# Kernel tuning notes

Measured on AMD Instinct MI355X. Metric: run time of the kernel, lower is better.

The kernel has to match this reference:

```python
import jax, jax.numpy as jnp
import numpy as np

B, K, T = 8192, 6, 30
HID, GRU_H, INTENT = 256, 256, 32


def setup_inputs() -> dict:
    key = jax.random.key(0)
    ks = jax.random.split(key, 11)
    s = lambda fan: 1.0 / np.sqrt(fan)
    return {
        "context": jax.random.normal(ks[0], (B, HID), jnp.float32),
        "goals": jax.random.normal(ks[1], (B, K, 2), jnp.float32),
        "intent_emb": jax.random.normal(ks[2], (B, INTENT), jnp.float32),
        "W_h0": jax.random.normal(ks[3], (GRU_H, HID + 2 + INTENT), jnp.float32) * s(HID + 34),
        "b_h0": jax.random.normal(ks[4], (GRU_H,), jnp.float32) * s(HID + 34),
        "W_ih": jax.random.normal(ks[5], (3 * GRU_H, 2), jnp.float32) * s(GRU_H),
        "W_hh": jax.random.normal(ks[6], (3 * GRU_H, GRU_H), jnp.float32) * s(GRU_H),
        "b_ih": jax.random.normal(ks[7], (3 * GRU_H,), jnp.float32) * s(GRU_H),
        "b_hh": jax.random.normal(ks[8], (3 * GRU_H,), jnp.float32) * s(GRU_H),
        "W_out": jax.random.normal(ks[9], (2, GRU_H), jnp.float32) * s(GRU_H),
        "b_out": jax.random.normal(ks[10], (2,), jnp.float32) * s(GRU_H),
    }


def reference(context, goals, intent_emb, W_h0, b_h0, W_ih, W_hh, b_ih, b_hh, W_out, b_out):
    Bq, Kq, _ = goals.shape
    H = W_hh.shape[1]
    # Fold modes into batch: init input is [context, goal_k, intent] per mode.
    ctx = jnp.broadcast_to(context[:, None, :], (Bq, Kq, context.shape[-1]))
    emb = jnp.broadcast_to(intent_emb[:, None, :], (Bq, Kq, intent_emb.shape[-1]))
    init_in = jnp.concatenate([ctx, goals, emb], axis=-1).reshape(Bq * Kq, -1)
    h0 = init_in @ W_h0.T + b_h0                       # (BK, H)
    pos0 = jnp.zeros((Bq * Kq, 2), dtype=context.dtype)

    def step(carry, _):
        h, prev = carry
        gi = prev @ W_ih.T + b_ih                      # (BK, 3H)
        gh = h @ W_hh.T + b_hh                         # (BK, 3H)
        i_r, i_z, i_n = jnp.split(gi, 3, axis=-1)
        h_r, h_z, h_n = jnp.split(gh, 3, axis=-1)
        r = jax.nn.sigmoid(i_r + h_r)
        z = jax.nn.sigmoid(i_z + h_z)
        n = jnp.tanh(i_n + r * h_n)
        h_new = (1.0 - z) * n + z * h
        delta = h_new @ W_out.T + b_out                # (BK, 2)
        pos = prev + delta
        return (h_new, pos), pos

    _, preds = jax.lax.scan(step, (h0, pos0), None, length=T)  # (T, BK, 2)
    preds = preds.transpose(1, 0, 2).reshape(Bq, Kq, T, 2)     # (B, K, T, 2)
    correction = goals - preds[:, :, -1, :]                    # (B, K, 2)
    scale = (jnp.arange(1, T + 1, dtype=preds.dtype) / T)      # (T,)
    return preds + correction[:, :, None, :] * scale[None, None, :, None]
```

## Files before the change

kernel.cpp:

```cpp
#include <hip/hip_runtime.h>


typedef __attribute__((ext_vector_type(8))) short short8;
typedef __bf16 bf16x8 __attribute__((ext_vector_type(8)));
typedef float f32x16 __attribute__((ext_vector_type(16)));
typedef float f32x4 __attribute__((ext_vector_type(4)));

#define HSTR 264
#define NSEQ_BLK 32
#define WHH3_ELEMS (24 * 16 * 64 * 8)
#define WH0_ELEMS (8 * 20 * 64 * 8)

static __device__ __forceinline__ unsigned short f2bf(float f) {
  unsigned u = __builtin_bit_cast(unsigned, f);
  u += 0x7fffu + ((u >> 16) & 1u);
  return (unsigned short)(u >> 16);
}
static __device__ __forceinline__ float bf2f(unsigned short h) {
  unsigned u = ((unsigned)h) << 16;
  return __builtin_bit_cast(float, u);
}
static __device__ __forceinline__ bf16x8 ldfrag(const unsigned short* p) {
  return __builtin_bit_cast(bf16x8, *(const short8*)p);
}
static __device__ __forceinline__ float fsig(float x) {
  return __builtin_amdgcn_rcpf(1.f + __builtin_amdgcn_exp2f(-1.44269504f * x));
}
static __device__ __forceinline__ float ftanh(float x) {
  return 1.f - 2.f * __builtin_amdgcn_rcpf(1.f + __builtin_amdgcn_exp2f(2.88539008f * x));
}
static __device__ __forceinline__ float dpp16sum(float x) {
  x += __builtin_bit_cast(float, __builtin_amdgcn_update_dpp(0, __builtin_bit_cast(int, x), 0xB1, 0xF, 0xF, true));
  x += __builtin_bit_cast(float, __builtin_amdgcn_update_dpp(0, __builtin_bit_cast(int, x), 0x4E, 0xF, 0xF, true));
  x += __builtin_bit_cast(float, __builtin_amdgcn_update_dpp(0, __builtin_bit_cast(int, x), 0x141, 0xF, 0xF, true));
  x += __builtin_bit_cast(float, __builtin_amdgcn_update_dpp(0, __builtin_bit_cast(int, x), 0x140, 0xF, 0xF, true));
  return x;
}
static __device__ __forceinline__ void bar_lgkm() {
  asm volatile("s_waitcnt lgkmcnt(0)\n\ts_barrier" ::: "memory");
}

__global__ void prep_whh3_k(const float* __restrict__ Whh, unsigned short* __restrict__ Whhp3) {
  int i = blockIdx.x * 256 + threadIdx.x;
  if (i >= WHH3_ELEMS) return;
  int j = i & 7;
  int lane = (i >> 3) & 63;
  int rest = i >> 9;
  int ks = rest & 15;
  int sw = rest >> 4;
  int g = sw >> 3, w = sw & 7;
  int row = g * 256 + w * 32 + (lane & 31);
  int k = ks * 16 + ((lane >> 5) << 3) + j;
  Whhp3[i] = f2bf(Whh[row * 256 + k]);
}

__global__ void prep_wh0_k(const float* __restrict__ Wh0, unsigned short* __restrict__ Wh0p) {
  int i = blockIdx.x * 256 + threadIdx.x;
  if (i >= WH0_ELEMS) return;
  int j = i & 7;
  int lane = (i >> 3) & 63;
  int rest = i >> 9;
  int ks = rest % 20;
  int nt = rest / 20;
  int row = nt * 32 + (lane & 31);
  int k = ks * 16 + ((lane >> 5) << 3) + j;
  float v = (k < 290) ? Wh0[row * 290 + k] : 0.f;
  Wh0p[i] = f2bf(v);
}

__global__ void prep_gp_k(const float* __restrict__ bih, const float* __restrict__ bhh,
                          const float* __restrict__ Wih, const float* __restrict__ Wout,
                          float* __restrict__ gpo) {
  int n = threadIdx.x;
  gpo[n * 12 + 0]  = bih[n] + bhh[n];
  gpo[n * 12 + 1]  = bih[n + 256] + bhh[n + 256];
  gpo[n * 12 + 2]  = bih[n + 512];
  gpo[n * 12 + 3]  = bhh[n + 512];
  gpo[n * 12 + 4]  = Wih[n * 2 + 0];
  gpo[n * 12 + 5]  = Wih[n * 2 + 1];
  gpo[n * 12 + 6]  = Wih[(n + 256) * 2 + 0];
  gpo[n * 12 + 7]  = Wih[(n + 256) * 2 + 1];
  gpo[n * 12 + 8]  = Wih[(n + 512) * 2 + 0];
  gpo[n * 12 + 9]  = Wih[(n + 512) * 2 + 1];
  gpo[n * 12 + 10] = Wout[n];
  gpo[n * 12 + 11] = Wout[256 + n];
}

__global__ __launch_bounds__(512, 2) void gru_main_k(
    const float* __restrict__ ctx, const float* __restrict__ goals,
    const float* __restrict__ emb, const float* __restrict__ bh0,
    const float* __restrict__ bout,
    const unsigned short* __restrict__ Wh0p,
    const unsigned short* __restrict__ Whhp3,
    const float* __restrict__ gp,
    float* __restrict__ out) {
  __shared__ __align__(16) unsigned short wNl[8 * 16 * 64 * 8];
  __shared__ __align__(16) unsigned short Hb[NSEQ_BLK * HSTR];
  __shared__ __align__(16) float dpart[16 * NSEQ_BLK * 2];
  __shared__ __align__(16) float posL[NSEQ_BLK * 2];

  const int tid = threadIdx.x;
  const int w = tid >> 6;
  const int l = tid & 63;
  const int l31 = l & 31;
  const int grp = l >> 5;
  const int seq0 = blockIdx.x * NSEQ_BLK;
  const int n0 = w * 32 + l31;

  {
    const short8* wsrc = (const short8*)(Whhp3 + 131072);
    short8* wdst = (short8*)wNl;
    for (int i = tid; i < 8192; i += 512) wdst[i] = wsrc[i];
  }
  bf16x8 wR[16], wZ[16];
#pragma unroll
  for (int ks = 0; ks < 16; ++ks) {
    wR[ks] = ldfrag(&Whhp3[(((0 * 8 + w) * 16 + ks) * 64 + l) * 8]);
    wZ[ks] = ldfrag(&Whhp3[(((1 * 8 + w) * 16 + ks) * 64 + l) * 8]);
  }

  f32x16 acc0 = f32x16{};
  unsigned short* As = Hb;
  for (int cc = 0; cc < 2; ++cc) {
    for (int i = tid; i < NSEQ_BLK * 160; i += 512) {
      int row = i / 160;
      int col = i - row * 160;
      int d = cc * 160 + col;
      int s = seq0 + row;
      int b = s / 6;
      float v;
      if (d < 256)      v = ctx[b * 256 + d];
      else if (d < 258) v = goals[s * 2 + (d - 256)];
      else if (d < 290) v = emb[b * 32 + (d - 258)];
      else              v = 0.f;
      As[row * 176 + col] = f2bf(v);
    }
    __syncthreads();
    for (int ks = 0; ks < 10; ++ks) {
      bf16x8 bf = ldfrag(&Wh0p[((w * 20 + cc * 10 + ks) * 64 + l) * 8]);
      bf16x8 af = ldfrag(&As[l31 * 176 + ks * 16 + grp * 8]);
      acc0 = __builtin_amdgcn_mfma_f32_32x32x16_bf16(af, bf, acc0, 0, 0, 0);
    }
    __syncthreads();
  }
  {
    float b0 = bh0[n0];
#pragma unroll
    for (int r = 0; r < 16; ++r) {
      int row = (r & 3) + 8 * (r >> 2) + 4 * grp;
      Hb[row * HSTR + n0] = f2bf(acc0[r] + b0);
    }
  }
  if (tid < 2 * NSEQ_BLK) posL[tid] = 0.f;

  float brr, bzz, bin_, bhn, wr0, wr1, wz0, wz1, wn0, wn1, wo0, wo1;
  {
    f32x4 g0 = *(const f32x4*)&gp[n0 * 12];
    f32x4 g1 = *(const f32x4*)&gp[n0 * 12 + 4];
    f32x4 g2 = *(const f32x4*)&gp[n0 * 12 + 8];
    brr = g0[0]; bzz = g0[1]; bin_ = g0[2]; bhn = g0[3];
    wr0 = g1[0]; wr1 = g1[1]; wz0 = g1[2]; wz1 = g1[3];
    wn0 = g2[0]; wn1 = g2[1]; wo0 = g2[2]; wo1 = g2[3];
  }
  const float bo0 = bout[0], bo1 = bout[1];
  __syncthreads();

  for (int t = 0; t < 30; ++t) {
    f32x16 ar = f32x16{}, az = f32x16{}, an = f32x16{};

#pragma unroll
    for (int ks = 0; ks < 16; ++ks) {
      bf16x8 af = ldfrag(&Hb[l31 * HSTR + ks * 16 + grp * 8]);
      bf16x8 bN = ldfrag(&wNl[((w * 16 + ks) * 64 + l) * 8]);
      ar = __builtin_amdgcn_mfma_f32_32x32x16_bf16(af, wR[ks], ar, 0, 0, 0);
      az = __builtin_amdgcn_mfma_f32_32x32x16_bf16(af, wZ[ks], az, 0, 0, 0);
      an = __builtin_amdgcn_mfma_f32_32x32x16_bf16(af, bN, an, 0, 0, 0);
    }
    bar_lgkm();

#pragma unroll
    for (int q2 = 0; q2 < 4; ++q2) {
      int sb = 8 * q2 + 4 * grp;
      f32x4 xyA = *(const f32x4*)&posL[sb * 2];
      f32x4 xyB = *(const f32x4*)&posL[sb * 2 + 4];
#pragma unroll
      for (int e = 0; e < 4; ++e) {
        int r = 4 * q2 + e;
        int s = sb + e;
        float x = (e == 0) ? xyA[0] : (e == 1) ? xyA[2] : (e == 2) ? xyB[0] : xyB[2];
        float y = (e == 0) ? xyA[1] : (e == 1) ? xyA[3] : (e == 2) ? xyB[1] : xyB[3];
        int ha = s * HSTR + n0;
        float h = bf2f(Hb[ha]);
        float rg = fsig(ar[r] + brr + x * wr0 + y * wr1);
        float zg = fsig(az[r] + bzz + x * wz0 + y * wz1);
        float ng = ftanh(fmaf(rg, an[r] + bhn, fmaf(x, wn0, fmaf(y, wn1, bin_))));
        float hnew = fmaf(zg, h - ng, ng);
        Hb[ha] = f2bf(hnew);
        float dx = dpp16sum(hnew * wo0);
        float dy = dpp16sum(hnew * wo1);
        if ((l & 15) == 0) {
          int p16 = w * 2 + ((l >> 4) & 1);
          dpart[(p16 * NSEQ_BLK + s) * 2]     = dx;
          dpart[(p16 * NSEQ_BLK + s) * 2 + 1] = dy;
        }
      }
    }
    bar_lgkm();

    if (tid < 2 * NSEQ_BLK) {
      int s = tid >> 1, c = tid & 1;
      float d = (c == 0) ? bo0 : bo1;
#pragma unroll
      for (int q = 0; q < 16; ++q) d += dpart[(q * NSEQ_BLK + s) * 2 + c];
      float p = posL[tid] + d;
      posL[tid] = p;
      out[((seq0 + s) * 30 + t) * 2 + c] = p;
    }
  }
}

__global__ void corr_k(float* __restrict__ out, const float* __restrict__ goals) {
  __shared__ float buf[240];
  int tid = threadIdx.x;
  int s0 = blockIdx.x * 4;
  float v = 0.f;
  if (tid < 240) { v = out[s0 * 60 + tid]; buf[tid] = v; }
  __syncthreads();
  if (tid < 240) {
    int sl = tid / 60;
    int rem = tid - sl * 60;
    int t = rem >> 1, c = rem & 1;
    float pT = buf[sl * 60 + 58 + c];
    float g = goals[(s0 + sl) * 2 + c];
    out[s0 * 60 + tid] = v + (g - pT) * ((float)(t + 1) * (1.f / 30.f));
  }
}

extern "C" void kernel_launch(void* const* d_in, const int* in_sizes, int n_in,
                              void* d_out, int out_size, void* d_ws, size_t ws_size,
                              hipStream_t stream) {
  (void)in_sizes; (void)n_in; (void)out_size; (void)ws_size;
  const float* ctx  = (const float*)d_in[0];
  const float* goals= (const float*)d_in[1];
  const float* emb  = (const float*)d_in[2];
  const float* Wh0  = (const float*)d_in[3];
  const float* bh0  = (const float*)d_in[4];
  const float* Wih  = (const float*)d_in[5];
  const float* Whh  = (const float*)d_in[6];
  const float* bih  = (const float*)d_in[7];
  const float* bhh  = (const float*)d_in[8];
  const float* Wout = (const float*)d_in[9];
  const float* bout = (const float*)d_in[10];
  float* out = (float*)d_out;

  unsigned short* Whhp3 = (unsigned short*)d_ws;
  unsigned short* Wh0p  = (unsigned short*)((char*)d_ws + 393216);
  float* gpo = (float*)((char*)d_ws + 393216 + 163840);

  hipLaunchKernelGGL(prep_whh3_k, dim3(768), dim3(256), 0, stream, Whh, Whhp3);
  hipLaunchKernelGGL(prep_wh0_k, dim3(320), dim3(256), 0, stream, Wh0, Wh0p);
  hipLaunchKernelGGL(prep_gp_k, dim3(1), dim3(256), 0, stream, bih, bhh, Wih, Wout, gpo);
  hipLaunchKernelGGL(gru_main_k, dim3(1536), dim3(512), 0, stream,
                     ctx, goals, emb, bh0, bout, Wh0p, Whhp3, gpo, out);
  hipLaunchKernelGGL(corr_k, dim3(12288), dim3(256), 0, stream, out, goals);
}
```

Baseline: 985.1 us.

## Ping-pong two sequence tiles per block to overlap MFMA with gate math

Each block now handles two 32-sequence tiles with double-buffered hidden state, dpart and position buffers. The recurrent GEMM for one tile is interleaved with the gate and elementwise phase of the other, hiding MFMA latency behind transcendental math. R and Z weights are read from global/L2 each step instead of being held in registers, most N weight slices stay in LDS, and the fp32 hidden state is kept in registers rather than re-read as bf16. The grid is halved, and occupancy and LDS pressure change as a result.

```diff
diff --git a/kernel.cpp b/kernel.cpp
--- a/kernel.cpp
+++ b/kernel.cpp
@@ -7,7 +7,8 @@
 typedef float f32x4 __attribute__((ext_vector_type(4)));
 
 #define HSTR 264
-#define NSEQ_BLK 32
+#define NSEQ 32
+#define WNL_SLICES 14
 #define WHH3_ELEMS (24 * 16 * 64 * 8)
 #define WH0_ELEMS (8 * 20 * 64 * 8)
 
@@ -15,10 +16,6 @@
   unsigned u = __builtin_bit_cast(unsigned, f);
   u += 0x7fffu + ((u >> 16) & 1u);
   return (unsigned short)(u >> 16);
-}
-static __device__ __forceinline__ float bf2f(unsigned short h) {
-  unsigned u = ((unsigned)h) << 16;
-  return __builtin_bit_cast(float, u);
 }
 static __device__ __forceinline__ bf16x8 ldfrag(const unsigned short* p) {
   return __builtin_bit_cast(bf16x8, *(const short8*)p);
@@ -94,64 +91,77 @@
     const unsigned short* __restrict__ Whhp3,
     const float* __restrict__ gp,
     float* __restrict__ out) {
-  __shared__ __align__(16) unsigned short wNl[8 * 16 * 64 * 8];
-  __shared__ __align__(16) unsigned short Hb[NSEQ_BLK * HSTR];
-  __shared__ __align__(16) float dpart[16 * NSEQ_BLK * 2];
-  __shared__ __align__(16) float posL[NSEQ_BLK * 2];
+  __shared__ __align__(16) unsigned short wNl[8 * WNL_SLICES * 64 * 8];
+  __shared__ __align__(16) unsigned short HbA[NSEQ * HSTR];
+  __shared__ __align__(16) unsigned short HbB[NSEQ * HSTR];
+  __shared__ __align__(16) float dpartA[16 * NSEQ * 2];
+  __shared__ __align__(16) float dpartB[16 * NSEQ * 2];
+  __shared__ __align__(16) float posA[NSEQ * 2];
+  __shared__ __align__(16) float posB[NSEQ * 2];
 
   const int tid = threadIdx.x;
   const int w = tid >> 6;
   const int l = tid & 63;
   const int l31 = l & 31;
   const int grp = l >> 5;
-  const int seq0 = blockIdx.x * NSEQ_BLK;
+  const int seq0 = blockIdx.x * (2 * NSEQ);
   const int n0 = w * 32 + l31;
 
   {
-    const short8* wsrc = (const short8*)(Whhp3 + 131072);
     short8* wdst = (short8*)wNl;
-    for (int i = tid; i < 8192; i += 512) wdst[i] = wsrc[i];
-  }
-  bf16x8 wR[16], wZ[16];
-#pragma unroll
-  for (int ks = 0; ks < 16; ++ks) {
-    wR[ks] = ldfrag(&Whhp3[(((0 * 8 + w) * 16 + ks) * 64 + l) * 8]);
-    wZ[ks] = ldfrag(&Whhp3[(((1 * 8 + w) * 16 + ks) * 64 + l) * 8]);
-  }
-
-  f32x16 acc0 = f32x16{};
-  unsigned short* As = Hb;
-  for (int cc = 0; cc < 2; ++cc) {
-    for (int i = tid; i < NSEQ_BLK * 160; i += 512) {
-      int row = i / 160;
-      int col = i - row * 160;
-      int d = cc * 160 + col;
-      int s = seq0 + row;
-      int b = s / 6;
-      float v;
-      if (d < 256)      v = ctx[b * 256 + d];
-      else if (d < 258) v = goals[s * 2 + (d - 256)];
-      else if (d < 290) v = emb[b * 32 + (d - 258)];
-      else              v = 0.f;
-      As[row * 176 + col] = f2bf(v);
-    }
-    __syncthreads();
-    for (int ks = 0; ks < 10; ++ks) {
-      bf16x8 bf = ldfrag(&Wh0p[((w * 20 + cc * 10 + ks) * 64 + l) * 8]);
-      bf16x8 af = ldfrag(&As[l31 * 176 + ks * 16 + grp * 8]);
-      acc0 = __builtin_amdgcn_mfma_f32_32x32x16_bf16(af, bf, acc0, 0, 0, 0);
-    }
-    __syncthreads();
-  }
+    const short8* wsrc = (const short8*)Whhp3;
+    for (int f = tid; f < 8 * WNL_SLICES * 64; f += 512) {
+      int ll = f & 63;
+      int t2 = f >> 6;
+      int ks = t2 % WNL_SLICES;
+      int ww = t2 / WNL_SLICES;
+      wdst[f] = wsrc[((16 + ww) * 16 + ks) * 64 + ll];
+    }
+  }
+
+  auto phase0 = [&](unsigned short* Hb, int sBase, f32x16& acc0) {
+    unsigned short* As = Hb;
+    for (int cc = 0; cc < 2; ++cc) {
+      for (int i = tid; i < NSEQ * 160; i += 512) {
+        int row = i / 160;
+        int col = i - row * 160;
+        int d = cc * 160 + col;
+        int s = sBase + row;
+        int b = s / 6;
+        float v;
+        if (d < 256)      v = ctx[b * 256 + d];
+        else if (d < 258) v = goals[s * 2 + (d - 256)];
+        else if (d < 290) v = emb[b * 32 + (d - 258)];
+        else              v = 0.f;
+        As[row * 176 + col] = f2bf(v);
+      }
+      __syncthreads();
+      for (int ks = 0; ks < 10; ++ks) {
+        bf16x8 bf = ldfrag(&Wh0p[((w * 20 + cc * 10 + ks) * 64 + l) * 8]);
+        bf16x8 af = ldfrag(&As[l31 * 176 + ks * 16 + grp * 8]);
+        acc0 = __builtin_amdgcn_mfma_f32_32x32x16_bf16(af, bf, acc0, 0, 0, 0);
+      }
+      __syncthreads();
+    }
+  };
+
+  f32x16 acc0A = f32x16{}, acc0B = f32x16{};
+  phase0(HbA, seq0, acc0A);
+  phase0(HbB, seq0 + NSEQ, acc0B);
+
+  float hA[16], hB[16];
   {
     float b0 = bh0[n0];
 #pragma unroll
     for (int r = 0; r < 16; ++r) {
       int row = (r & 3) + 8 * (r >> 2) + 4 * grp;
-      Hb[row * HSTR + n0] = f2bf(acc0[r] + b0);
-    }
-  }
-  if (tid < 2 * NSEQ_BLK) posL[tid] = 0.f;
+      hA[r] = acc0A[r] + b0;
+      hB[r] = acc0B[r] + b0;
+      HbA[row * HSTR + n0] = f2bf(hA[r]);
+      HbB[row * HSTR + n0] = f2bf(hB[r]);
+    }
+  }
+  if (tid < 2 * NSEQ) { posA[tid] = 0.f; posB[tid] = 0.f; }
 
   float brr, bzz, bin_, bhn, wr0, wr1, wz0, wz1, wn0, wn1, wo0, wo1;
   {
@@ -165,19 +175,28 @@
   const float bo0 = bout[0], bo1 = bout[1];
   __syncthreads();
 
-  for (int t = 0; t < 30; ++t) {
-    f32x16 ar = f32x16{}, az = f32x16{}, an = f32x16{};
-
+  const unsigned short* wRb = &Whhp3[((w * 16) * 64 + l) * 8];
+  const unsigned short* wZb = &Whhp3[(((8 + w) * 16) * 64 + l) * 8];
+  const unsigned short* wNg = &Whhp3[(((16 + w) * 16) * 64 + l) * 8];
+
+  auto kloop = [&](const unsigned short* Hb, f32x16& ar, f32x16& az, f32x16& an) {
+    ar = f32x16{}; az = f32x16{}; an = f32x16{};
 #pragma unroll
     for (int ks = 0; ks < 16; ++ks) {
       bf16x8 af = ldfrag(&Hb[l31 * HSTR + ks * 16 + grp * 8]);
-      bf16x8 bN = ldfrag(&wNl[((w * 16 + ks) * 64 + l) * 8]);
-      ar = __builtin_amdgcn_mfma_f32_32x32x16_bf16(af, wR[ks], ar, 0, 0, 0);
-      az = __builtin_amdgcn_mfma_f32_32x32x16_bf16(af, wZ[ks], az, 0, 0, 0);
+      bf16x8 bR = ldfrag(&wRb[ks * 512]);
+      bf16x8 bZ = ldfrag(&wZb[ks * 512]);
+      bf16x8 bN = (ks < WNL_SLICES)
+          ? ldfrag(&wNl[((w * WNL_SLICES + ks) * 64 + l) * 8])
+          : ldfrag(&wNg[ks * 512]);
+      ar = __builtin_amdgcn_mfma_f32_32x32x16_bf16(af, bR, ar, 0, 0, 0);
+      az = __builtin_amdgcn_mfma_f32_32x32x16_bf16(af, bZ, az, 0, 0, 0);
       an = __builtin_amdgcn_mfma_f32_32x32x16_bf16(af, bN, an, 0, 0, 0);
     }
-    bar_lgkm();
-
+  };
+
+  auto phaseB = [&](const f32x16& ar, const f32x16& az, const f32x16& an,
+                    float* posL, unsigned short* Hb, float* dpart, float (&h)[16]) {
 #pragma unroll
     for (int q2 = 0; q2 < 4; ++q2) {
       int sb = 8 * q2 + 4 * grp;
@@ -189,34 +208,51 @@
         int s = sb + e;
         float x = (e == 0) ? xyA[0] : (e == 1) ? xyA[2] : (e == 2) ? xyB[0] : xyB[2];
         float y = (e == 0) ? xyA[1] : (e == 1) ? xyA[3] : (e == 2) ? xyB[1] : xyB[3];
-        int ha = s * HSTR + n0;
-        float h = bf2f(Hb[ha]);
         float rg = fsig(ar[r] + brr + x * wr0 + y * wr1);
         float zg = fsig(az[r] + bzz + x * wz0 + y * wz1);
         float ng = ftanh(fmaf(rg, an[r] + bhn, fmaf(x, wn0, fmaf(y, wn1, bin_))));
-        float hnew = fmaf(zg, h - ng, ng);
-        Hb[ha] = f2bf(hnew);
+        float hnew = fmaf(zg, h[r] - ng, ng);
+        h[r] = hnew;
+        Hb[s * HSTR + n0] = f2bf(hnew);
         float dx = dpp16sum(hnew * wo0);
         float dy = dpp16sum(hnew * wo1);
         if ((l & 15) == 0) {
           int p16 = w * 2 + ((l >> 4) & 1);
-          dpart[(p16 * NSEQ_BLK + s) * 2]     = dx;
-          dpart[(p16 * NSEQ_BLK + s) * 2 + 1] = dy;
+          dpart[(p16 * NSEQ + s) * 2]     = dx;
+          dpart[(p16 * NSEQ + s) * 2 + 1] = dy;
         }
       }
     }
+  };
+
+  auto phaseC = [&](float* posL, float* dpart, int sBase, int st, int tbase) {
+    int tt = tid - tbase;
+    if (tt >= 0 && tt < 2 * NSEQ) {
+      int s = tt >> 1, c = tt & 1;
+      float d = (c == 0) ? bo0 : bo1;
+#pragma unroll
+      for (int q = 0; q < 16; ++q) d += dpart[(q * NSEQ + s) * 2 + c];
+      float p = posL[tt] + d;
+      posL[tt] = p;
+      out[((sBase + s) * 30 + st) * 2 + c] = p;
+    }
+  };
+
+  f32x16 arA, azA, anA, arB, azB, anB;
+  kloop(HbA, arA, azA, anA);
+
+#pragma unroll 1
+  for (int t = 0; t < 30; ++t) {
+    kloop(HbB, arB, azB, anB);
+    if (t > 0) phaseC(posB, dpartB, seq0 + NSEQ, t - 1, 64);
+    phaseB(arA, azA, anA, posA, HbA, dpartA, hA);
     bar_lgkm();
-
-    if (tid < 2 * NSEQ_BLK) {
-      int s = tid >> 1, c = tid & 1;
-      float d = (c == 0) ? bo0 : bo1;
-#pragma unroll
-      for (int q = 0; q < 16; ++q) d += dpart[(q * NSEQ_BLK + s) * 2 + c];
-      float p = posL[tid] + d;
-      posL[tid] = p;
-      out[((seq0 + s) * 30 + t) * 2 + c] = p;
-    }
-  }
+    if (t < 29) kloop(HbA, arA, azA, anA);
+    phaseC(posA, dpartA, seq0, t, 0);
+    phaseB(arB, azB, anB, posB, HbB, dpartB, hB);
+    bar_lgkm();
+  }
+  phaseC(posB, dpartB, seq0 + NSEQ, 29, 64);
 }
 
 __global__ void corr_k(float* __restrict__ out, const float* __restrict__ goals) {
@@ -260,7 +296,7 @@
   hipLaunchKernelGGL(prep_whh3_k, dim3(768), dim3(256), 0, stream, Whh, Whhp3);
   hipLaunchKernelGGL(prep_wh0_k, dim3(320), dim3(256), 0, stream, Wh0, Wh0p);
   hipLaunchKernelGGL(prep_gp_k, dim3(1), dim3(256), 0, stream, bih, bhh, Wih, Wout, gpo);
-  hipLaunchKernelGGL(gru_main_k, dim3(1536), dim3(512), 0, stream,
+  hipLaunchKernelGGL(gru_main_k, dim3(768), dim3(512), 0, stream,
                      ctx, goals, emb, bh0, bout, Wh0p, Whhp3, gpo, out);
   hipLaunchKernelGGL(corr_k, dim3(12288), dim3(256), 0, stream, out, goals);
 }
```

Result: slower. 2.695 ms (+173.6%).

## Stream R/Z weights from global and shrink LDS weight cache for occupancy

Applied to the files above, without the earlier changes.

Stops holding the R and Z gate weight fragments in registers and reloads them from global/L2 on every timestep. The N-gate weights are now only partly cached in LDS (7 of 16 k-slices); the rest are read from global. Launch bounds go from 2 to 4 blocks per CU to raise occupancy. The trade-off is that each step of the recurrent loop now issues many global loads, which may be latency-bound. Loop unrolling is also reduced to limit register pressure.

```diff
diff --git a/kernel.cpp b/kernel.cpp
--- a/kernel.cpp
+++ b/kernel.cpp
@@ -8,6 +8,7 @@
 
 #define HSTR 264
 #define NSEQ_BLK 32
+#define WNL_SLICES 7
 #define WHH3_ELEMS (24 * 16 * 64 * 8)
 #define WH0_ELEMS (8 * 20 * 64 * 8)
 
@@ -86,7 +87,7 @@
   gpo[n * 12 + 11] = Wout[256 + n];
 }
 
-__global__ __launch_bounds__(512, 2) void gru_main_k(
+__global__ __launch_bounds__(512, 4) void gru_main_k(
     const float* __restrict__ ctx, const float* __restrict__ goals,
     const float* __restrict__ emb, const float* __restrict__ bh0,
     const float* __restrict__ bout,
@@ -94,7 +95,7 @@
     const unsigned short* __restrict__ Whhp3,
     const float* __restrict__ gp,
     float* __restrict__ out) {
-  __shared__ __align__(16) unsigned short wNl[8 * 16 * 64 * 8];
+  __shared__ __align__(16) unsigned short wNl[8 * WNL_SLICES * 64 * 8];
   __shared__ __align__(16) unsigned short Hb[NSEQ_BLK * HSTR];
   __shared__ __align__(16) float dpart[16 * NSEQ_BLK * 2];
   __shared__ __align__(16) float posL[NSEQ_BLK * 2];
@@ -108,40 +109,42 @@
   const int n0 = w * 32 + l31;
 
   {
-    const short8* wsrc = (const short8*)(Whhp3 + 131072);
     short8* wdst = (short8*)wNl;
-    for (int i = tid; i < 8192; i += 512) wdst[i] = wsrc[i];
-  }
-  bf16x8 wR[16], wZ[16];
-#pragma unroll
-  for (int ks = 0; ks < 16; ++ks) {
-    wR[ks] = ldfrag(&Whhp3[(((0 * 8 + w) * 16 + ks) * 64 + l) * 8]);
-    wZ[ks] = ldfrag(&Whhp3[(((1 * 8 + w) * 16 + ks) * 64 + l) * 8]);
+    const short8* wsrc = (const short8*)Whhp3;
+    for (int f = tid; f < 8 * WNL_SLICES * 64; f += 512) {
+      int ll = f & 63;
+      int t2 = f >> 6;
+      int ks = t2 % WNL_SLICES;
+      int ww = t2 / WNL_SLICES;
+      wdst[f] = wsrc[((16 + ww) * 16 + ks) * 64 + ll];
+    }
   }
 
   f32x16 acc0 = f32x16{};
-  unsigned short* As = Hb;
-  for (int cc = 0; cc < 2; ++cc) {
-    for (int i = tid; i < NSEQ_BLK * 160; i += 512) {
-      int row = i / 160;
-      int col = i - row * 160;
-      int d = cc * 160 + col;
-      int s = seq0 + row;
-      int b = s / 6;
-      float v;
-      if (d < 256)      v = ctx[b * 256 + d];
-      else if (d < 258) v = goals[s * 2 + (d - 256)];
-      else if (d < 290) v = emb[b * 32 + (d - 258)];
-      else              v = 0.f;
-      As[row * 176 + col] = f2bf(v);
-    }
-    __syncthreads();
-    for (int ks = 0; ks < 10; ++ks) {
-      bf16x8 bf = ldfrag(&Wh0p[((w * 20 + cc * 10 + ks) * 64 + l) * 8]);
-      bf16x8 af = ldfrag(&As[l31 * 176 + ks * 16 + grp * 8]);
-      acc0 = __builtin_amdgcn_mfma_f32_32x32x16_bf16(af, bf, acc0, 0, 0, 0);
-    }
-    __syncthreads();
+  {
+    unsigned short* As = Hb;
+    for (int cc = 0; cc < 2; ++cc) {
+      for (int i = tid; i < NSEQ_BLK * 160; i += 512) {
+        int row = i / 160;
+        int col = i - row * 160;
+        int d = cc * 160 + col;
+        int s = seq0 + row;
+        int b = s / 6;
+        float v;
+        if (d < 256)      v = ctx[b * 256 + d];
+        else if (d < 258) v = goals[s * 2 + (d - 256)];
+        else if (d < 290) v = emb[b * 32 + (d - 258)];
+        else              v = 0.f;
+        As[row * 176 + col] = f2bf(v);
+      }
+      __syncthreads();
+      for (int ks = 0; ks < 10; ++ks) {
+        bf16x8 bf = ldfrag(&Wh0p[((w * 20 + cc * 10 + ks) * 64 + l) * 8]);
+        bf16x8 af = ldfrag(&As[l31 * 176 + ks * 16 + grp * 8]);
+        acc0 = __builtin_amdgcn_mfma_f32_32x32x16_bf16(af, bf, acc0, 0, 0, 0);
+      }
+      __syncthreads();
+    }
   }
   {
     float b0 = bh0[n0];
@@ -165,15 +168,24 @@
   const float bo0 = bout[0], bo1 = bout[1];
   __syncthreads();
 
+  const unsigned short* wRb = &Whhp3[((w * 16) * 64 + l) * 8];
+  const unsigned short* wZb = &Whhp3[(((8 + w) * 16) * 64 + l) * 8];
+  const unsigned short* wNg = &Whhp3[(((16 + w) * 16) * 64 + l) * 8];
+
+#pragma unroll 1
   for (int t = 0; t < 30; ++t) {
     f32x16 ar = f32x16{}, az = f32x16{}, an = f32x16{};
 
-#pragma unroll
+#pragma unroll 2
     for (int ks = 0; ks < 16; ++ks) {
       bf16x8 af = ldfrag(&Hb[l31 * HSTR + ks * 16 + grp * 8]);
-      bf16x8 bN = ldfrag(&wNl[((w * 16 + ks) * 64 + l) * 8]);
-      ar = __builtin_amdgcn_mfma_f32_32x32x16_bf16(af, wR[ks], ar, 0, 0, 0);
-      az = __builtin_amdgcn_mfma_f32_32x32x16_bf16(af, wZ[ks], az, 0, 0, 0);
+      bf16x8 bR = ldfrag(&wRb[ks * 512]);
+      bf16x8 bZ = ldfrag(&wZb[ks * 512]);
+      bf16x8 bN = (ks < WNL_SLICES)
+          ? ldfrag(&wNl[((w * WNL_SLICES + ks) * 64 + l) * 8])
+          : ldfrag(&wNg[ks * 512]);
+      ar = __builtin_amdgcn_mfma_f32_32x32x16_bf16(af, bR, ar, 0, 0, 0);
+      az = __builtin_amdgcn_mfma_f32_32x32x16_bf16(af, bZ, az, 0, 0, 0);
       an = __builtin_amdgcn_mfma_f32_32x32x16_bf16(af, bN, an, 0, 0, 0);
     }
     bar_lgkm();
```

Measured after the change: 1.054 ms. 1.07x slower.
